# Kernel tuning notes

Hardware: AMD Instinct MI355X
Metric: run time of the kernel (lower is better)

The kernel has to match this reference:

```python
import jax, jax.numpy as jnp
import numpy as np

K = 8192          # num_embeddings
D = 256           # embedding_dim
DECAY = 0.95
EPS = 1e-05
COMMIT = 0.25


def setup_inputs() -> dict:
    key = jax.random.key(0)
    k1, k2, k3 = jax.random.split(key, 3)
    x = jax.random.normal(k1, (32, D, 32, 32), dtype=jnp.float32)
    codebook = jax.random.uniform(k2, (K, D), dtype=jnp.float32,
                                  minval=-1.0 / K, maxval=1.0 / K)
    ema_count = jnp.zeros((K,), dtype=jnp.float32)
    ema_weight = jax.random.normal(k3, (K, D), dtype=jnp.float32)
    return {"x": x, "codebook": codebook, "ema_count": ema_count,
            "ema_weight": ema_weight}


def reference(x, codebook, ema_count, ema_weight):
    b, c, h, w = x.shape
    inputs = jnp.transpose(x, (0, 2, 3, 1))          # [B,H,W,C]
    flat = inputs.reshape(-1, c)                     # [N,C], N=B*H*W
    n = flat.shape[0]

    # squared euclidean distances: ||z||^2 + ||e||^2 - 2 z.e
    distances = (jnp.sum(flat * flat, axis=1, keepdims=True)
                 + jnp.sum(codebook * codebook, axis=1)
                 - 2.0 * flat @ codebook.T)          # [N,K]
    idx = jnp.argmin(distances, axis=1)              # [N]

    # one-hot @ codebook == gather
    quantized = codebook[idx].reshape(inputs.shape)  # [B,H,W,C]

    # EMA codebook update (training branch, no-grad in torch)
    counts = jax.ops.segment_sum(jnp.ones((n,), flat.dtype), idx,
                                 num_segments=K)     # encodings.sum(0)
    new_count = ema_count * DECAY + (1.0 - DECAY) * counts
    new_count = (new_count + EPS) / (n + K * EPS) * n
    dw = jax.ops.segment_sum(flat, idx, num_segments=K)  # encodings.T @ flat
    new_weight = ema_weight * DECAY + (1.0 - DECAY) * dw
    new_codebook = new_weight / new_count[:, None]

    e_loss = COMMIT * jnp.mean((jax.lax.stop_gradient(quantized) - inputs) ** 2)
    quantized_st = inputs + jax.lax.stop_gradient(quantized - inputs)

    indices = idx.reshape(b, h * w)
    return (e_loss,
            jnp.transpose(quantized_st, (0, 3, 1, 2)),
            indices,
            new_count, new_weight, new_codebook)
```

## Files before the change

### kernel.cpp

```cpp
#include <hip/hip_runtime.h>
#include <stdint.h>

#define N_TOK 32768
#define DIM   256
#define KCB   8192
#define HWSZ  1024

#define WS_FLATB   0u
#define WS_CBB     4194304u
#define WS_A32     5242880u
#define WS_B32     5275648u
#define WS_IDX     5283840u
#define WS_CAND    5316608u
#define WS_ICNT    5840896u
#define WS_CUR     5849088u
#define WS_OFFS    5857280u
#define WS_PERM    5865472u
#define WS_LPART   5898240u
#define WS_DW      5914624u
#define WS_TOTAL   8011776u
#define WS_MEMSET_LEN 16384u

#define O_LOSS 0u
#define O_Q    1u
#define O_IDX  8388609u
#define O_CNT  8421377u
#define O_W    8429569u
#define O_CB   10526721u

typedef __attribute__((ext_vector_type(8))) short bf16x8;
typedef __attribute__((ext_vector_type(4))) float f32x4;

__device__ __forceinline__ void g2lds16(const void* gp, void* lp){
  __builtin_amdgcn_global_load_lds(
      (const __attribute__((address_space(1))) void*)gp,
      (__attribute__((address_space(3))) void*)lp, 16, 0, 0);
}

__device__ __forceinline__ unsigned short f2b(float f){
  unsigned u = __float_as_uint(f);
  return (unsigned short)((u + 0x7FFFu + ((u >> 16) & 1u)) >> 16);
}

__device__ __forceinline__ unsigned umin2(unsigned a, unsigned b){ return a < b ? a : b; }
__device__ __forceinline__ unsigned umax2(unsigned a, unsigned b){ return a > b ? a : b; }

__device__ __forceinline__ float np_pairwise_sq(const float* __restrict__ p, int stride){
  #pragma clang fp contract(off)
  float h[2];
  #pragma unroll
  for (int half = 0; half < 2; half++){
    const float* q = p + half * 128 * stride;
    float r[8];
    #pragma unroll
    for (int j = 0; j < 8; j++){ float z = q[j * stride]; r[j] = z * z; }
    for (int i = 8; i < 128; i += 8){
      #pragma unroll
      for (int j = 0; j < 8; j++){ float z = q[(i + j) * stride]; r[j] = r[j] + z * z; }
    }
    h[half] = ((r[0] + r[1]) + (r[2] + r[3])) + ((r[4] + r[5]) + (r[6] + r[7]));
  }
  return h[0] + h[1];
}

__global__ void k_prep(const float* __restrict__ x, const float* __restrict__ cb,
                       unsigned short* __restrict__ flatB, unsigned short* __restrict__ cbB,
                       float* __restrict__ a32, float* __restrict__ b32)
{
  __shared__ float tile[64][65];
  const int bx = blockIdx.x;
  const int t = threadIdx.x;
  if (bx < 2048){
    const int b = bx >> 6, ct = (bx >> 4) & 3, ht = bx & 15;
    const int c0 = ct * 64, hw0 = ht * 64;
    const int rr = t >> 4, cc4 = (t & 15) * 4;
    #pragma unroll
    for (int j = 0; j < 4; j++){
      const int crow = rr + j * 16;
      float4 v = *(const float4*)(x + ((size_t)(b * 256 + c0 + crow) << 10) + hw0 + cc4);
      tile[crow][cc4] = v.x; tile[crow][cc4+1] = v.y; tile[crow][cc4+2] = v.z; tile[crow][cc4+3] = v.w;
    }
    __syncthreads();
    #pragma unroll
    for (int j = 0; j < 4; j++){
      const int hwrow = rr + j * 16;
      ushort4 o = { f2b(tile[cc4][hwrow]), f2b(tile[cc4+1][hwrow]),
                    f2b(tile[cc4+2][hwrow]), f2b(tile[cc4+3][hwrow]) };
      *(ushort4*)(flatB + ((size_t)(b * 1024 + hw0 + hwrow) << 8) + c0 + cc4) = o;
    }
  } else if (bx < 4096){
    const int g = (bx - 2048) * 256 + t;
    float4 v = *(const float4*)(cb + (size_t)g * 4);
    ushort4 o = { f2b(v.x), f2b(v.y), f2b(v.z), f2b(v.w) };
    *(ushort4*)(cbB + (size_t)g * 4) = o;
  } else {
    const int g = (bx - 4096) * 256 + t;
    if (g < N_TOK){
      int b = g >> 10, hw = g & 1023;
      a32[g] = np_pairwise_sq(x + (size_t)b * 262144 + hw, 1024);
    } else {
      int k2 = g - N_TOK;
      b32[k2] = np_pairwise_sq(cb + (size_t)k2 * 256, 1);
    }
  }
}

__launch_bounds__(256, 2)
__global__ void k_dist(const unsigned short* __restrict__ flatB,
                       const unsigned short* __restrict__ cbB,
                       const float* __restrict__ b32,
                       int* __restrict__ cand)
{
  __shared__ __align__(16) unsigned short A1[128 * 128];
  __shared__ __align__(16) unsigned short Bs[2][128 * 64];

  const int tid = threadIdx.x;
  const int bx = blockIdx.x;
  const int tt = bx >> 1, h = bx & 1;
  const int tok0 = tt * 128;
  const int wv = tid >> 6, lane = tid & 63;
  const int wy = wv >> 1, wx = wv & 1;
  const int l4 = lane >> 4, lm = lane & 15;

  const unsigned short* fB = flatB + (size_t)tok0 * 256;
  const unsigned short* cB = cbB + (size_t)h * 4096 * 256;

  {
    const int r = lane >> 4, p = lane & 15;
    #pragma unroll
    for (int j = 0; j < 8; j++){
      const int row = wv * 32 + j * 4 + r;
      const int gc = p ^ (row & 15);
      g2lds16((const char*)fB + (size_t)row * 512 + (gc << 4),
              (char*)A1 + (wv * 32 + j * 4) * 256);
    }
    unsigned short* A2 = &Bs[0][0];
    #pragma unroll
    for (int j = 0; j < 8; j++){
      const int row = wv * 32 + j * 4 + r;
      const int gc = p ^ (row & 15);
      g2lds16((const char*)fB + (size_t)row * 512 + 256 + (gc << 4),
              (char*)A2 + (wv * 32 + j * 4) * 256);
    }
  }
  __syncthreads();

  bf16x8 a2[4][4];
  {
    const unsigned short* A2 = &Bs[0][0];
    #pragma unroll
    for (int ks4 = 0; ks4 < 4; ks4++)
      #pragma unroll
      for (int ii = 0; ii < 4; ii++){
        const int m = wy * 64 + ii * 16 + lm;
        const int c = ks4 * 4 + l4;
        a2[ks4][ii] = *(const bf16x8*)((const char*)A2 + m * 256 + ((c ^ (m & 15)) << 4));
      }
  }
  __syncthreads();

  unsigned aoff[4][4];
  #pragma unroll
  for (int kg = 0; kg < 4; kg++)
    #pragma unroll
    for (int ii = 0; ii < 4; ii++){
      const int m = wy * 64 + ii * 16 + lm;
      const int ca = kg * 4 + l4;
      aoff[kg][ii] = (unsigned)(m * 256 + ((ca ^ (m & 15)) << 4));
    }
  unsigned boff[2][2][4];
  #pragma unroll
  for (int buf = 0; buf < 2; buf++)
    #pragma unroll
    for (int ks2 = 0; ks2 < 2; ks2++)
      #pragma unroll
      for (int jj = 0; jj < 4; jj++){
        const int n = wx * 64 + jj * 16 + lm;
        const int c2 = ks2 * 4 + l4;
        boff[buf][ks2][jj] = (unsigned)(buf * 16384 + n * 128 + ((c2 ^ (n & 7)) << 4));
      }
  const char* gBj[4];
  unsigned dstj[4];
  {
    const int r8 = lane >> 3, p = lane & 7;
    #pragma unroll
    for (int j = 0; j < 4; j++){
      const int row = wv * 32 + j * 8 + r8;
      const int gc = p ^ (row & 7);
      gBj[j] = (const char*)cB + (size_t)row * 512 + (gc << 4);
      dstj[j] = (unsigned)((wv * 32 + j * 8) * 128);
    }
  }

  auto stageB = [&](int S2){
    const int ss = S2 & 3, cc = S2 >> 2;
    const int buf = (S2 & 1) * 16384;
    const size_t soff = (size_t)(cc * 65536 + ss * 128);
    #pragma unroll
    for (int j = 0; j < 4; j++)
      g2lds16(gBj[j] + soff, (char*)Bs + buf + dstj[j]);
  };

  unsigned k1[16], k2[16];
  #pragma unroll
  for (int i = 0; i < 16; i++){ k1[i] = 0xFFFFFFFFu; k2[i] = 0xFFFFFFFFu; }

  f32x4 acc[4][4];
  float bn125[4];

  stageB(0);
  __syncthreads();

  for (int c = 0; c < 32; c++){
    #pragma unroll
    for (int s = 0; s < 4; s++){
      const int S = c * 4 + s;
      if (S + 1 < 128) stageB(S + 1);
      if (s == 0){
        #pragma unroll
        for (int jj = 0; jj < 4; jj++)
          bn125[jj] = b32[h * 4096 + c * 128 + wx * 64 + jj * 16 + lm] + 0.125f;
        #pragma unroll
        for (int ii = 0; ii < 4; ii++)
          #pragma unroll
          for (int jj = 0; jj < 4; jj++)
            acc[ii][jj] = (f32x4){0.f, 0.f, 0.f, 0.f};
      }
      #pragma unroll
      for (int ks2 = 0; ks2 < 2; ks2++){
        const int kg = s * 2 + ks2;
        bf16x8 bf[4], af[4];
        #pragma unroll
        for (int jj = 0; jj < 4; jj++)
          bf[jj] = *(const bf16x8*)((const char*)Bs + boff[s & 1][ks2][jj]);
        if (kg < 4){
          #pragma unroll
          for (int ii = 0; ii < 4; ii++)
            af[ii] = *(const bf16x8*)((const char*)A1 + aoff[kg][ii]);
        } else {
          #pragma unroll
          for (int ii = 0; ii < 4; ii++) af[ii] = a2[kg - 4][ii];
        }
        #pragma unroll
        for (int ii = 0; ii < 4; ii++)
          #pragma unroll
          for (int jj = 0; jj < 4; jj++)
            acc[ii][jj] = __builtin_amdgcn_mfma_f32_16x16x32_bf16(af[ii], bf[jj], acc[ii][jj], 0, 0, 0);
      }
      if (s == 3){
        unsigned pk[4];
        #pragma unroll
        for (int jj = 0; jj < 4; jj++) pk[jj] = (unsigned)((c << 2) | jj);
        #pragma unroll
        for (int ii = 0; ii < 4; ii++){
          #pragma unroll
          for (int r = 0; r < 4; r++){
            const int rk = ii * 4 + r;
            unsigned kb[4];
            #pragma unroll
            for (int jj = 0; jj < 4; jj++){
              const float v = fmaf(-2.f, acc[ii][jj][r], bn125[jj]);
              kb[jj] = (__float_as_uint(v) & 0xFFFFFF80u) | pk[jj];
            }
            const unsigned lo01 = umin2(kb[0], kb[1]), hi01 = umax2(kb[0], kb[1]);
            const unsigned lo23 = umin2(kb[2], kb[3]), hi23 = umax2(kb[2], kb[3]);
            const unsigned s1 = umin2(lo01, lo23);
            const unsigned s2 = umin2(umax2(lo01, lo23), umin2(hi01, hi23));
            const unsigned t = umax2(k1[rk], s1);
            k1[rk] = umin2(k1[rk], s1);
            k2[rk] = umin2(umin2(k2[rk], t), s2);
          }
        }
      }
      __syncthreads();
    }
  }

  const unsigned colbase = (unsigned)(wx * 64 + lm);
  auto fin = [colbase](unsigned key)->unsigned {
    const float v125 = __uint_as_float(key & 0xFFFFFF80u);
    int qi = (int)(v125 * 4194304.f);
    qi = qi < 0 ? 0 : (qi > 0xFFFFF ? 0xFFFFF : qi);
    const unsigned cc = (key >> 2) & 31u, jj = key & 3u;
    return ((unsigned)qi << 12) | (cc * 128u + jj * 16u + colbase);
  };
  unsigned* red = (unsigned*)&A1[0];
  #pragma unroll
  for (int rk = 0; rk < 16; rk++){
    const int srow = wy * 64 + (rk >> 2) * 16 + l4 * 4 + (rk & 3);
    red[srow * 64 + wx * 32 + lm * 2 + 0] = fin(k1[rk]);
    red[srow * 64 + wx * 32 + lm * 2 + 1] = fin(k2[rk]);
  }
  __syncthreads();
  if (tid < 128){
    unsigned best[8];
    #pragma unroll
    for (int j = 0; j < 8; j++) best[j] = 0xFFFFFFFFu;
    for (int i = 0; i < 64; i++){
      unsigned k = red[tid * 64 + i];
      if (k < best[7]){
        best[7] = k;
        #pragma unroll
        for (int j = 7; j > 0; j--){
          if (best[j] < best[j-1]){ unsigned tmp = best[j]; best[j] = best[j-1]; best[j-1] = tmp; }
        }
      }
    }
    const size_t base = ((size_t)(tok0 + tid) * 2 + h) * 8;
    #pragma unroll
    for (int j = 0; j < 8; j++) cand[base + j] = h * 4096 + (int)(best[j] & 0xFFFu);
  }
}

__global__ void k_pick(const float* __restrict__ x, const float* __restrict__ cb,
                       const float* __restrict__ a32, const float* __restrict__ b32,
                       const int* __restrict__ cand, int* __restrict__ idx,
                       int* __restrict__ icnt, float* __restrict__ out_idx,
                       float* __restrict__ outq, double* __restrict__ lpart)
{
  __shared__ double wred[4];
  const int gt = blockIdx.x * 256 + threadIdx.x;
  const int wid = gt >> 6;
  const int lane = gt & 63;
  const int tq = lane & 3, cg = lane >> 2;
  const int n = wid * 4 + tq;
  const int b = n >> 10, hw = n & 1023;

  const size_t xbase = (((size_t)(b * 256 + cg * 16)) << 10) + hw;
  float z[16];
  #pragma unroll
  for (int j = 0; j < 16; j++) z[j] = x[xbase + ((size_t)j << 10)];

  const float an = a32[n];
  float bestd = 3.4e38f; int besti = 0x7fffffff;
  for (int j = 0; j < 16; j++){
    const int ci = cand[(size_t)n * 16 + j];
    if (ci < 0 || ci >= KCB) continue;
    const float* ep = cb + (size_t)ci * DIM + cg * 16;
    float4 e0 = *(const float4*)(ep + 0);
    float4 e1 = *(const float4*)(ep + 4);
    float4 e2 = *(const float4*)(ep + 8);
    float4 e3 = *(const float4*)(ep + 12);
    double se = (double)z[0]*e0.x + (double)z[1]*e0.y + (double)z[2]*e0.z + (double)z[3]*e0.w
              + (double)z[4]*e1.x + (double)z[5]*e1.y + (double)z[6]*e1.z + (double)z[7]*e1.w
              + (double)z[8]*e2.x + (double)z[9]*e2.y + (double)z[10]*e2.z + (double)z[11]*e2.w
              + (double)z[12]*e3.x + (double)z[13]*e3.y + (double)z[14]*e3.z + (double)z[15]*e3.w;
    se += __shfl_xor(se, 4, 64);
    se += __shfl_xor(se, 8, 64);
    se += __shfl_xor(se, 16, 64);
    se += __shfl_xor(se, 32, 64);
    const float A = an + b32[ci];
    const float d32 = (float)((double)A - 2.0 * se);
    if (d32 < bestd || (d32 == bestd && ci < besti)){ bestd = d32; besti = ci; }
  }

  double p = 0.0;
  {
    const float* ep = cb + (size_t)besti * DIM + cg * 16;
    float4 e0 = *(const float4*)(ep + 0);
    float4 e1 = *(const float4*)(ep + 4);
    float4 e2 = *(const float4*)(ep + 8);
    float4 e3 = *(const float4*)(ep + 12);
    float q[16] = { e0.x, e0.y, e0.z, e0.w, e1.x, e1.y, e1.z, e1.w,
                    e2.x, e2.y, e2.z, e2.w, e3.x, e3.y, e3.z, e3.w };
    #pragma unroll
    for (int j = 0; j < 16; j++){
      const float qd = q[j] - z[j];
      outq[xbase + ((size_t)j << 10)] = z[j] + qd;
      p += (double)(qd * qd);
    }
  }
  #pragma unroll
  for (int o = 32; o > 0; o >>= 1) p += __shfl_down(p, o, 64);
  if ((threadIdx.x & 63) == 0) wred[threadIdx.x >> 6] = p;

  if (cg == 0){
    idx[n] = besti;
    atomicAdd(icnt + besti, 1);
    out_idx[n] = (float)besti;
  }
  __syncthreads();
  if (threadIdx.x == 0) lpart[blockIdx.x] = (wred[0] + wred[1]) + (wred[2] + wred[3]);
}

__global__ void k_perm(const int* __restrict__ idx, const int* __restrict__ icnt,
                       int* __restrict__ cur, int* __restrict__ perm,
                       int* __restrict__ offs)
{
  __shared__ int offs_l[8192];
  __shared__ int sums[256];
  const int tid = threadIdx.x;
  int loc[32];
  int s = 0;
  #pragma unroll
  for (int i = 0; i < 32; i++){ loc[i] = s; s += icnt[tid * 32 + i]; }
  sums[tid] = s;
  #pragma unroll
  for (int off = 1; off < 256; off <<= 1){
    __syncthreads();
    const int add = (tid >= off) ? sums[tid - off] : 0;
    __syncthreads();
    sums[tid] += add;
  }
  __syncthreads();
  const int pre = (tid == 0) ? 0 : sums[tid - 1];
  #pragma unroll
  for (int i = 0; i < 32; i++) offs_l[tid * 32 + i] = pre + loc[i];
  if (blockIdx.x == 0){
    #pragma unroll
    for (int i = 0; i < 32; i++) offs[tid * 32 + i] = pre + loc[i];
  }
  __syncthreads();
  const int t = blockIdx.x * 256 + tid;
  const int code = idx[t];
  const int slot = atomicAdd(cur + code, 1);
  perm[offs_l[code] + slot] = t;
}

__global__ void k_dwf(const unsigned short* __restrict__ flatB,
                      const int* __restrict__ offs, const int* __restrict__ icnt,
                      const int* __restrict__ perm,
                      const float* __restrict__ ema_w, const float* __restrict__ ema_count,
                      const double* __restrict__ lpart, float* __restrict__ out)
{
  const int k = blockIdx.x;
  const int c = threadIdx.x;
  const int start = offs[k], cnt = icnt[k];
  float s = 0.f;
  for (int i = 0; i < cnt; i++){
    const int n = perm[start + i];
    s += __uint_as_float(((unsigned)flatB[((size_t)n << 8) + c]) << 16);
  }
  float ct1 = ema_count[k] * 0.95f;
  float ct2 = 0.05f * (float)cnt;
  float sc  = ct1 + ct2;
  float sc2 = sc + 1e-5f;
  const float DEN = (float)(32768.0 + 8192.0 * 1e-5);
  float nc = (sc2 / DEN) * 32768.0f;
  if (c == 0) out[O_CNT + k] = nc;
  {
    #pragma clang fp contract(off)
    const int t = k * 256 + c;
    float w = ema_w[t];
    float t1 = w * 0.95f;
    float t2 = 0.05f * s;
    float nw = t1 + t2;
    out[O_W + t]  = nw;
    out[O_CB + t] = nw / nc;
  }
  if (k == 0){
    __shared__ double sred[256];
    double ls = 0.0;
    for (int i = c; i < 2048; i += 256) ls += lpart[i];
    sred[c] = ls;
    __syncthreads();
    for (int off = 128; off > 0; off >>= 1){
      if (c < off) sred[c] += sred[c + off];
      __syncthreads();
    }
    if (c == 0) out[O_LOSS] = 0.25f * (float)(sred[0] / 8388608.0);
  }
}

extern "C" void kernel_launch(void* const* d_in, const int* in_sizes, int n_in,
                              void* d_out, int out_size, void* d_ws, size_t ws_size,
                              hipStream_t stream)
{
  const float* x         = (const float*)d_in[0];
  const float* cb        = (const float*)d_in[1];
  const float* ema_count = (const float*)d_in[2];
  const float* ema_w     = (const float*)d_in[3];
  float* out = (float*)d_out;
  float* ws  = (float*)d_ws;

  unsigned short* flatB = (unsigned short*)(ws + WS_FLATB);
  unsigned short* cbB   = (unsigned short*)(ws + WS_CBB);
  float*  a32    = ws + WS_A32;
  float*  b32    = ws + WS_B32;
  int*    idxp   = (int*)(ws + WS_IDX);
  int*    candp  = (int*)(ws + WS_CAND);
  int*    icnt   = (int*)(ws + WS_ICNT);
  int*    curp   = (int*)(ws + WS_CUR);
  int*    offs   = (int*)(ws + WS_OFFS);
  int*    permp  = (int*)(ws + WS_PERM);
  double* lpart  = (double*)(ws + WS_LPART);

  (void)hipMemsetAsync(ws + WS_ICNT, 0, (size_t)WS_MEMSET_LEN * sizeof(float), stream);

  k_prep <<<4256, 256, 0, stream>>>(x, cb, flatB, cbB, a32, b32);
  k_dist <<<512,  256, 0, stream>>>(flatB, cbB, b32, candp);
  k_pick <<<2048, 256, 0, stream>>>(x, cb, a32, b32, candp, idxp, icnt,
                                    out + O_IDX, out + O_Q, lpart);
  k_perm <<<128,  256, 0, stream>>>(idxp, icnt, curp, permp, offs);
  k_dwf  <<<8192, 256, 0, stream>>>(flatB, offs, icnt, permp, ema_w, ema_count,
                                    lpart, out);
}
```

Measured before the change: 384.3 us.

## Halve distance-kernel token tile and fuse token norms into transpose prep

The distance kernel now handles 64 tokens per block instead of 128, doubling the grid to 1024 blocks and raising launch bounds to 3 waves per SIMD to improve occupancy on the many-CU GPU. The cost is that each codebook tile is reused by half as many tokens, so codebook traffic from L2 doubles. Separately, the prep kernel transposes a full 256-channel by 16-token tile and computes the token squared norms from LDS. This replaces the earlier strided global reads of x, keeping the same pairwise summation order.

New measurement: 427.9 us. 11.3% more time.

```diff
diff --git a/kernel.cpp b/kernel.cpp
--- a/kernel.cpp
+++ b/kernel.cpp
@@ -17,7 +17,6 @@
 #define WS_OFFS    5857280u
 #define WS_PERM    5865472u
 #define WS_LPART   5898240u
-#define WS_DW      5914624u
 #define WS_TOTAL   8011776u
 #define WS_MEMSET_LEN 16384u
 
@@ -67,26 +66,46 @@
                        unsigned short* __restrict__ flatB, unsigned short* __restrict__ cbB,
                        float* __restrict__ a32, float* __restrict__ b32)
 {
-  __shared__ float tile[64][65];
   const int bx = blockIdx.x;
   const int t = threadIdx.x;
   if (bx < 2048){
-    const int b = bx >> 6, ct = (bx >> 4) & 3, ht = bx & 15;
-    const int c0 = ct * 64, hw0 = ht * 64;
-    const int rr = t >> 4, cc4 = (t & 15) * 4;
+    __shared__ float tile[256][17];
+    const int b = bx >> 6, ht = bx & 63;
+    const int hw0 = ht * 16;
+    const int n0 = b * 1024 + hw0;
+    const int wv = t >> 6, lane = t & 63;
+    {
+      const int cr = lane >> 2, hq = (lane & 3) * 4;
+      #pragma unroll
+      for (int j = 0; j < 4; j++){
+        const int c = wv * 64 + j * 16 + cr;
+        float4 v = *(const float4*)(x + ((size_t)(b * 256 + c) << 10) + hw0 + hq);
+        tile[c][hq] = v.x; tile[c][hq+1] = v.y; tile[c][hq+2] = v.z; tile[c][hq+3] = v.w;
+      }
+    }
+    __syncthreads();
     #pragma unroll
     for (int j = 0; j < 4; j++){
-      const int crow = rr + j * 16;
-      float4 v = *(const float4*)(x + ((size_t)(b * 256 + c0 + crow) << 10) + hw0 + cc4);
-      tile[crow][cc4] = v.x; tile[crow][cc4+1] = v.y; tile[crow][cc4+2] = v.z; tile[crow][cc4+3] = v.w;
-    }
-    __syncthreads();
-    #pragma unroll
-    for (int j = 0; j < 4; j++){
-      const int hwrow = rr + j * 16;
-      ushort4 o = { f2b(tile[cc4][hwrow]), f2b(tile[cc4+1][hwrow]),
-                    f2b(tile[cc4+2][hwrow]), f2b(tile[cc4+3][hwrow]) };
-      *(ushort4*)(flatB + ((size_t)(b * 1024 + hw0 + hwrow) << 8) + c0 + cc4) = o;
+      const int tok = wv * 4 + j;
+      ushort4 o = { f2b(tile[lane*4+0][tok]), f2b(tile[lane*4+1][tok]),
+                    f2b(tile[lane*4+2][tok]), f2b(tile[lane*4+3][tok]) };
+      *(ushort4*)(flatB + ((size_t)(n0 + tok) << 8) + lane * 4) = o;
+    }
+    if (t < 16){
+      #pragma clang fp contract(off)
+      float h[2];
+      #pragma unroll
+      for (int half = 0; half < 2; half++){
+        float r[8];
+        #pragma unroll
+        for (int j = 0; j < 8; j++){ float z = tile[half*128 + j][t]; r[j] = z * z; }
+        for (int i = 8; i < 128; i += 8){
+          #pragma unroll
+          for (int j = 0; j < 8; j++){ float z = tile[half*128 + i + j][t]; r[j] = r[j] + z * z; }
+        }
+        h[half] = ((r[0] + r[1]) + (r[2] + r[3])) + ((r[4] + r[5]) + (r[6] + r[7]));
+      }
+      a32[n0 + t] = h[0] + h[1];
     }
   } else if (bx < 4096){
     const int g = (bx - 2048) * 256 + t;
@@ -95,29 +114,23 @@
     *(ushort4*)(cbB + (size_t)g * 4) = o;
   } else {
     const int g = (bx - 4096) * 256 + t;
-    if (g < N_TOK){
-      int b = g >> 10, hw = g & 1023;
-      a32[g] = np_pairwise_sq(x + (size_t)b * 262144 + hw, 1024);
-    } else {
-      int k2 = g - N_TOK;
-      b32[k2] = np_pairwise_sq(cb + (size_t)k2 * 256, 1);
-    }
-  }
-}
-
-__launch_bounds__(256, 2)
+    if (g < KCB) b32[g] = np_pairwise_sq(cb + (size_t)g * 256, 1);
+  }
+}
+
+__launch_bounds__(256, 3)
 __global__ void k_dist(const unsigned short* __restrict__ flatB,
                        const unsigned short* __restrict__ cbB,
                        const float* __restrict__ b32,
                        int* __restrict__ cand)
 {
-  __shared__ __align__(16) unsigned short A1[128 * 128];
+  __shared__ __align__(16) unsigned short A1[64 * 128];
   __shared__ __align__(16) unsigned short Bs[2][128 * 64];
 
   const int tid = threadIdx.x;
   const int bx = blockIdx.x;
   const int tt = bx >> 1, h = bx & 1;
-  const int tok0 = tt * 128;
+  const int tok0 = tt * 64;
   const int wv = tid >> 6, lane = tid & 63;
   const int wy = wv >> 1, wx = wv & 1;
   const int l4 = lane >> 4, lm = lane & 15;
@@ -128,43 +141,43 @@
   {
     const int r = lane >> 4, p = lane & 15;
     #pragma unroll
-    for (int j = 0; j < 8; j++){
-      const int row = wv * 32 + j * 4 + r;
+    for (int j = 0; j < 4; j++){
+      const int row = wv * 16 + j * 4 + r;
       const int gc = p ^ (row & 15);
       g2lds16((const char*)fB + (size_t)row * 512 + (gc << 4),
-              (char*)A1 + (wv * 32 + j * 4) * 256);
+              (char*)A1 + (wv * 16 + j * 4) * 256);
     }
     unsigned short* A2 = &Bs[0][0];
     #pragma unroll
-    for (int j = 0; j < 8; j++){
-      const int row = wv * 32 + j * 4 + r;
+    for (int j = 0; j < 4; j++){
+      const int row = wv * 16 + j * 4 + r;
       const int gc = p ^ (row & 15);
       g2lds16((const char*)fB + (size_t)row * 512 + 256 + (gc << 4),
-              (char*)A2 + (wv * 32 + j * 4) * 256);
-    }
-  }
-  __syncthreads();
-
-  bf16x8 a2[4][4];
+              (char*)A2 + (wv * 16 + j * 4) * 256);
+    }
+  }
+  __syncthreads();
+
+  bf16x8 a2[4][2];
   {
     const unsigned short* A2 = &Bs[0][0];
     #pragma unroll
     for (int ks4 = 0; ks4 < 4; ks4++)
       #pragma unroll
-      for (int ii = 0; ii < 4; ii++){
-        const int m = wy * 64 + ii * 16 + lm;
+      for (int ii = 0; ii < 2; ii++){
+        const int m = wy * 32 + ii * 16 + lm;
         const int c = ks4 * 4 + l4;
         a2[ks4][ii] = *(const bf16x8*)((const char*)A2 + m * 256 + ((c ^ (m & 15)) << 4));
       }
   }
   __syncthreads();
 
-  unsigned aoff[4][4];
+  unsigned aoff[4][2];
   #pragma unroll
   for (int kg = 0; kg < 4; kg++)
     #pragma unroll
-    for (int ii = 0; ii < 4; ii++){
-      const int m = wy * 64 + ii * 16 + lm;
+    for (int ii = 0; ii < 2; ii++){
+      const int m = wy * 32 + ii * 16 + lm;
       const int ca = kg * 4 + l4;
       aoff[kg][ii] = (unsigned)(m * 256 + ((ca ^ (m & 15)) << 4));
     }
@@ -201,11 +214,11 @@
       g2lds16(gBj[j] + soff, (char*)Bs + buf + dstj[j]);
   };
 
-  unsigned k1[16], k2[16];
-  #pragma unroll
-  for (int i = 0; i < 16; i++){ k1[i] = 0xFFFFFFFFu; k2[i] = 0xFFFFFFFFu; }
-
-  f32x4 acc[4][4];
+  unsigned k1[8], k2[8];
+  #pragma unroll
+  for (int i = 0; i < 8; i++){ k1[i] = 0xFFFFFFFFu; k2[i] = 0xFFFFFFFFu; }
+
+  f32x4 acc[2][4];
   float bn125[4];
 
   stageB(0);
@@ -221,7 +234,7 @@
         for (int jj = 0; jj < 4; jj++)
           bn125[jj] = b32[h * 4096 + c * 128 + wx * 64 + jj * 16 + lm] + 0.125f;
         #pragma unroll
-        for (int ii = 0; ii < 4; ii++)
+        for (int ii = 0; ii < 2; ii++)
           #pragma unroll
           for (int jj = 0; jj < 4; jj++)
             acc[ii][jj] = (f32x4){0.f, 0.f, 0.f, 0.f};
@@ -229,20 +242,20 @@
       #pragma unroll
       for (int ks2 = 0; ks2 < 2; ks2++){
         const int kg = s * 2 + ks2;
-        bf16x8 bf[4], af[4];
+        bf16x8 bf[4], af[2];
         #pragma unroll
         for (int jj = 0; jj < 4; jj++)
           bf[jj] = *(const bf16x8*)((const char*)Bs + boff[s & 1][ks2][jj]);
         if (kg < 4){
           #pragma unroll
-          for (int ii = 0; ii < 4; ii++)
+          for (int ii = 0; ii < 2; ii++)
             af[ii] = *(const bf16x8*)((const char*)A1 + aoff[kg][ii]);
         } else {
           #pragma unroll
-          for (int ii = 0; ii < 4; ii++) af[ii] = a2[kg - 4][ii];
+          for (int ii = 0; ii < 2; ii++) af[ii] = a2[kg - 4][ii];
         }
         #pragma unroll
-        for (int ii = 0; ii < 4; ii++)
+        for (int ii = 0; ii < 2; ii++)
           #pragma unroll
           for (int jj = 0; jj < 4; jj++)
             acc[ii][jj] = __builtin_amdgcn_mfma_f32_16x16x32_bf16(af[ii], bf[jj], acc[ii][jj], 0, 0, 0);
@@ -252,7 +265,7 @@
         #pragma unroll
         for (int jj = 0; jj < 4; jj++) pk[jj] = (unsigned)((c << 2) | jj);
         #pragma unroll
-        for (int ii = 0; ii < 4; ii++){
+        for (int ii = 0; ii < 2; ii++){
           #pragma unroll
           for (int r = 0; r < 4; r++){
             const int rk = ii * 4 + r;
@@ -286,13 +299,13 @@
   };
   unsigned* red = (unsigned*)&A1[0];
   #pragma unroll
-  for (int rk = 0; rk < 16; rk++){
-    const int srow = wy * 64 + (rk >> 2) * 16 + l4 * 4 + (rk & 3);
+  for (int rk = 0; rk < 8; rk++){
+    const int srow = wy * 32 + (rk >> 2) * 16 + l4 * 4 + (rk & 3);
     red[srow * 64 + wx * 32 + lm * 2 + 0] = fin(k1[rk]);
     red[srow * 64 + wx * 32 + lm * 2 + 1] = fin(k2[rk]);
   }
   __syncthreads();
-  if (tid < 128){
+  if (tid < 64){
     unsigned best[8];
     #pragma unroll
     for (int j = 0; j < 8; j++) best[j] = 0xFFFFFFFFu;
@@ -487,8 +500,8 @@
 
   (void)hipMemsetAsync(ws + WS_ICNT, 0, (size_t)WS_MEMSET_LEN * sizeof(float), stream);
 
-  k_prep <<<4256, 256, 0, stream>>>(x, cb, flatB, cbB, a32, b32);
-  k_dist <<<512,  256, 0, stream>>>(flatB, cbB, b32, candp);
+  k_prep <<<4128, 256, 0, stream>>>(x, cb, flatB, cbB, a32, b32);
+  k_dist <<<1024, 256, 0, stream>>>(flatB, cbB, b32, candp);
   k_pick <<<2048, 256, 0, stream>>>(x, cb, a32, b32, candp, idxp, icnt,
                                     out + O_IDX, out + O_Q, lpart);
   k_perm <<<128,  256, 0, stream>>>(idxp, icnt, curp, permp, offs);
```

## Load codebook MFMA fragments directly from pre-tiled global layout, drop LDS staging

Applied to the files above, without the earlier changes.

The codebook is now stored in a fragment-tiled bf16 layout so k_dist can read B operands straight from global memory into registers, removing the double-buffered LDS staging and per-step barriers. The second half of the A tile is also loaded directly from global, and occupancy is raised to 3 blocks per SM. k_prep computes token norms from the shared transpose tile instead of a separate strided pass. The risk is that global/L2 latency for every B fragment is exposed without LDS reuse across waves, which doubles global traffic for B.

Result: slower. 652.5 us (+69.8%).

```diff
diff --git a/kernel.cpp b/kernel.cpp
--- a/kernel.cpp
+++ b/kernel.cpp
@@ -7,7 +7,7 @@
 #define HWSZ  1024
 
 #define WS_FLATB   0u
-#define WS_CBB     4194304u
+#define WS_CBT     4194304u
 #define WS_A32     5242880u
 #define WS_B32     5275648u
 #define WS_IDX     5283840u
@@ -17,7 +17,6 @@
 #define WS_OFFS    5857280u
 #define WS_PERM    5865472u
 #define WS_LPART   5898240u
-#define WS_DW      5914624u
 #define WS_TOTAL   8011776u
 #define WS_MEMSET_LEN 16384u
 
@@ -64,55 +63,71 @@
 }
 
 __global__ void k_prep(const float* __restrict__ x, const float* __restrict__ cb,
-                       unsigned short* __restrict__ flatB, unsigned short* __restrict__ cbB,
+                       unsigned short* __restrict__ flatB, unsigned short* __restrict__ cbT,
                        float* __restrict__ a32, float* __restrict__ b32)
 {
-  __shared__ float tile[64][65];
   const int bx = blockIdx.x;
   const int t = threadIdx.x;
   if (bx < 2048){
-    const int b = bx >> 6, ct = (bx >> 4) & 3, ht = bx & 15;
-    const int c0 = ct * 64, hw0 = ht * 64;
-    const int rr = t >> 4, cc4 = (t & 15) * 4;
+    __shared__ float tile[256][17];
+    const int b = bx >> 6, ht = bx & 63;
+    const int hw0 = ht * 16;
+    const int n0 = b * 1024 + hw0;
+    const int wv = t >> 6, lane = t & 63;
+    {
+      const int cr = lane >> 2, hq = (lane & 3) * 4;
+      #pragma unroll
+      for (int j = 0; j < 4; j++){
+        const int c = wv * 64 + j * 16 + cr;
+        float4 v = *(const float4*)(x + ((size_t)(b * 256 + c) << 10) + hw0 + hq);
+        tile[c][hq] = v.x; tile[c][hq+1] = v.y; tile[c][hq+2] = v.z; tile[c][hq+3] = v.w;
+      }
+    }
+    __syncthreads();
     #pragma unroll
     for (int j = 0; j < 4; j++){
-      const int crow = rr + j * 16;
-      float4 v = *(const float4*)(x + ((size_t)(b * 256 + c0 + crow) << 10) + hw0 + cc4);
-      tile[crow][cc4] = v.x; tile[crow][cc4+1] = v.y; tile[crow][cc4+2] = v.z; tile[crow][cc4+3] = v.w;
-    }
-    __syncthreads();
-    #pragma unroll
-    for (int j = 0; j < 4; j++){
-      const int hwrow = rr + j * 16;
-      ushort4 o = { f2b(tile[cc4][hwrow]), f2b(tile[cc4+1][hwrow]),
-                    f2b(tile[cc4+2][hwrow]), f2b(tile[cc4+3][hwrow]) };
-      *(ushort4*)(flatB + ((size_t)(b * 1024 + hw0 + hwrow) << 8) + c0 + cc4) = o;
+      const int tok = wv * 4 + j;
+      ushort4 o = { f2b(tile[lane*4+0][tok]), f2b(tile[lane*4+1][tok]),
+                    f2b(tile[lane*4+2][tok]), f2b(tile[lane*4+3][tok]) };
+      *(ushort4*)(flatB + ((size_t)(n0 + tok) << 8) + lane * 4) = o;
+    }
+    if (t < 16){
+      #pragma clang fp contract(off)
+      float h[2];
+      #pragma unroll
+      for (int half = 0; half < 2; half++){
+        float r[8];
+        #pragma unroll
+        for (int j = 0; j < 8; j++){ float z = tile[half*128 + j][t]; r[j] = z * z; }
+        for (int i = 8; i < 128; i += 8){
+          #pragma unroll
+          for (int j = 0; j < 8; j++){ float z = tile[half*128 + i + j][t]; r[j] = r[j] + z * z; }
+        }
+        h[half] = ((r[0] + r[1]) + (r[2] + r[3])) + ((r[4] + r[5]) + (r[6] + r[7]));
+      }
+      a32[n0 + t] = h[0] + h[1];
     }
   } else if (bx < 4096){
     const int g = (bx - 2048) * 256 + t;
+    const int k = g >> 6;
+    const int d0 = (g & 63) * 4;
     float4 v = *(const float4*)(cb + (size_t)g * 4);
     ushort4 o = { f2b(v.x), f2b(v.y), f2b(v.z), f2b(v.w) };
-    *(ushort4*)(cbB + (size_t)g * 4) = o;
+    const size_t toff = ((size_t)((k >> 4) * 32 + (d0 >> 3))) * 128 + (k & 15) * 8 + (d0 & 7);
+    *(ushort4*)(cbT + toff) = o;
   } else {
     const int g = (bx - 4096) * 256 + t;
-    if (g < N_TOK){
-      int b = g >> 10, hw = g & 1023;
-      a32[g] = np_pairwise_sq(x + (size_t)b * 262144 + hw, 1024);
-    } else {
-      int k2 = g - N_TOK;
-      b32[k2] = np_pairwise_sq(cb + (size_t)k2 * 256, 1);
-    }
-  }
-}
-
-__launch_bounds__(256, 2)
+    if (g < KCB) b32[g] = np_pairwise_sq(cb + (size_t)g * 256, 1);
+  }
+}
+
+__launch_bounds__(256, 3)
 __global__ void k_dist(const unsigned short* __restrict__ flatB,
-                       const unsigned short* __restrict__ cbB,
+                       const unsigned short* __restrict__ cbT,
                        const float* __restrict__ b32,
                        int* __restrict__ cand)
 {
   __shared__ __align__(16) unsigned short A1[128 * 128];
-  __shared__ __align__(16) unsigned short Bs[2][128 * 64];
 
   const int tid = threadIdx.x;
   const int bx = blockIdx.x;
@@ -123,7 +138,6 @@
   const int l4 = lane >> 4, lm = lane & 15;
 
   const unsigned short* fB = flatB + (size_t)tok0 * 256;
-  const unsigned short* cB = cbB + (size_t)h * 4096 * 256;
 
   {
     const int r = lane >> 4, p = lane & 15;
@@ -134,29 +148,17 @@
       g2lds16((const char*)fB + (size_t)row * 512 + (gc << 4),
               (char*)A1 + (wv * 32 + j * 4) * 256);
     }
-    unsigned short* A2 = &Bs[0][0];
-    #pragma unroll
-    for (int j = 0; j < 8; j++){
-      const int row = wv * 32 + j * 4 + r;
-      const int gc = p ^ (row & 15);
-      g2lds16((const char*)fB + (size_t)row * 512 + 256 + (gc << 4),
-              (char*)A2 + (wv * 32 + j * 4) * 256);
-    }
-  }
-  __syncthreads();
+  }
 
   bf16x8 a2[4][4];
-  {
-    const unsigned short* A2 = &Bs[0][0];
-    #pragma unroll
-    for (int ks4 = 0; ks4 < 4; ks4++)
-      #pragma unroll
-      for (int ii = 0; ii < 4; ii++){
-        const int m = wy * 64 + ii * 16 + lm;
-        const int c = ks4 * 4 + l4;
-        a2[ks4][ii] = *(const bf16x8*)((const char*)A2 + m * 256 + ((c ^ (m & 15)) << 4));
-      }
-  }
+  #pragma unroll
+  for (int ks4 = 0; ks4 < 4; ks4++)
+    #pragma unroll
+    for (int ii = 0; ii < 4; ii++){
+      const int m = wy * 64 + ii * 16 + lm;
+      const int dg = 16 + ks4 * 4 + l4;
+      a2[ks4][ii] = *(const bf16x8*)((const char*)fB + (size_t)m * 512 + dg * 16);
+    }
   __syncthreads();
 
   unsigned aoff[4][4];
@@ -168,38 +170,12 @@
       const int ca = kg * 4 + l4;
       aoff[kg][ii] = (unsigned)(m * 256 + ((ca ^ (m & 15)) << 4));
     }
-  unsigned boff[2][2][4];
-  #pragma unroll
-  for (int buf = 0; buf < 2; buf++)
-    #pragma unroll
-    for (int ks2 = 0; ks2 < 2; ks2++)
-      #pragma unroll
-      for (int jj = 0; jj < 4; jj++){
-        const int n = wx * 64 + jj * 16 + lm;
-        const int c2 = ks2 * 4 + l4;
-        boff[buf][ks2][jj] = (unsigned)(buf * 16384 + n * 128 + ((c2 ^ (n & 7)) << 4));
-      }
-  const char* gBj[4];
-  unsigned dstj[4];
-  {
-    const int r8 = lane >> 3, p = lane & 7;
-    #pragma unroll
-    for (int j = 0; j < 4; j++){
-      const int row = wv * 32 + j * 8 + r8;
-      const int gc = p ^ (row & 7);
-      gBj[j] = (const char*)cB + (size_t)row * 512 + (gc << 4);
-      dstj[j] = (unsigned)((wv * 32 + j * 8) * 128);
-    }
-  }
-
-  auto stageB = [&](int S2){
-    const int ss = S2 & 3, cc = S2 >> 2;
-    const int buf = (S2 & 1) * 16384;
-    const size_t soff = (size_t)(cc * 65536 + ss * 128);
-    #pragma unroll
-    for (int j = 0; j < 4; j++)
-      g2lds16(gBj[j] + soff, (char*)Bs + buf + dstj[j]);
-  };
+  const char* bj[4];
+  #pragma unroll
+  for (int jj = 0; jj < 4; jj++){
+    const int cg0 = h * 256 + wx * 4 + jj;
+    bj[jj] = (const char*)cbT + (size_t)cg0 * 8192 + lane * 16;
+  }
 
   unsigned k1[16], k2[16];
   #pragma unroll
@@ -208,31 +184,26 @@
   f32x4 acc[4][4];
   float bn125[4];
 
-  stageB(0);
-  __syncthreads();
-
   for (int c = 0; c < 32; c++){
+    const size_t cboff = (size_t)c << 16;
+    #pragma unroll
+    for (int jj = 0; jj < 4; jj++)
+      bn125[jj] = b32[h * 4096 + c * 128 + wx * 64 + jj * 16 + lm] + 0.125f;
+    #pragma unroll
+    for (int ii = 0; ii < 4; ii++)
+      #pragma unroll
+      for (int jj = 0; jj < 4; jj++)
+        acc[ii][jj] = (f32x4){0.f, 0.f, 0.f, 0.f};
+
     #pragma unroll
     for (int s = 0; s < 4; s++){
-      const int S = c * 4 + s;
-      if (S + 1 < 128) stageB(S + 1);
-      if (s == 0){
-        #pragma unroll
-        for (int jj = 0; jj < 4; jj++)
-          bn125[jj] = b32[h * 4096 + c * 128 + wx * 64 + jj * 16 + lm] + 0.125f;
-        #pragma unroll
-        for (int ii = 0; ii < 4; ii++)
-          #pragma unroll
-          for (int jj = 0; jj < 4; jj++)
-            acc[ii][jj] = (f32x4){0.f, 0.f, 0.f, 0.f};
-      }
       #pragma unroll
       for (int ks2 = 0; ks2 < 2; ks2++){
         const int kg = s * 2 + ks2;
         bf16x8 bf[4], af[4];
         #pragma unroll
         for (int jj = 0; jj < 4; jj++)
-          bf[jj] = *(const bf16x8*)((const char*)Bs + boff[s & 1][ks2][jj]);
+          bf[jj] = *(const bf16x8*)(bj[jj] + cboff + (unsigned)(kg << 10));
         if (kg < 4){
           #pragma unroll
           for (int ii = 0; ii < 4; ii++)
@@ -272,10 +243,10 @@
           }
         }
       }
-      __syncthreads();
-    }
-  }
-
+    }
+  }
+
+  __syncthreads();
   const unsigned colbase = (unsigned)(wx * 64 + lm);
   auto fin = [colbase](unsigned key)->unsigned {
     const float v125 = __uint_as_float(key & 0xFFFFFF80u);
@@ -474,7 +445,7 @@
   float* ws  = (float*)d_ws;
 
   unsigned short* flatB = (unsigned short*)(ws + WS_FLATB);
-  unsigned short* cbB   = (unsigned short*)(ws + WS_CBB);
+  unsigned short* cbT   = (unsigned short*)(ws + WS_CBT);
   float*  a32    = ws + WS_A32;
   float*  b32    = ws + WS_B32;
   int*    idxp   = (int*)(ws + WS_IDX);
@@ -487,8 +458,8 @@
 
   (void)hipMemsetAsync(ws + WS_ICNT, 0, (size_t)WS_MEMSET_LEN * sizeof(float), stream);
 
-  k_prep <<<4256, 256, 0, stream>>>(x, cb, flatB, cbB, a32, b32);
-  k_dist <<<512,  256, 0, stream>>>(flatB, cbB, b32, candp);
+  k_prep <<<4128, 256, 0, stream>>>(x, cb, flatB, cbT, a32, b32);
+  k_dist <<<512,  256, 0, stream>>>(flatB, cbT, b32, candp);
   k_pick <<<2048, 256, 0, stream>>>(x, cb, a32, b32, candp, idxp, icnt,
                                     out + O_IDX, out + O_Q, lpart);
   k_perm <<<128,  256, 0, stream>>>(idxp, icnt, curp, permp, offs);
```
